# Performance work log

Measured on AMD Instinct MI355X. Metric: run time of the kernel, lower is better.

The kernel has to match this reference:

```python
import jax, jax.numpy as jnp
import numpy as np

N_NODES = 20000
N_EDGES = 200000
N_GRAPHS = 128
EMB = 256
N_LAYERS = 4
NUM_ELEMENTS = 84
RBF_DIM = 10
RBF_CUTOFF = 8.0


def setup_inputs() -> dict:
    key = jax.random.key(0)
    ks = jax.random.split(key, 20)
    inp = {
        'x': jax.random.randint(ks[0], (N_NODES, 1), 0, NUM_ELEMENTS, dtype=jnp.int64) if jax.config.read('jax_enable_x64') else jax.random.randint(ks[0], (N_NODES, 1), 0, NUM_ELEMENTS).astype(jnp.int32),
        'src': jax.random.randint(ks[1], (N_EDGES,), 0, N_NODES).astype(jnp.int32),
        'dst': jax.random.randint(ks[2], (N_EDGES,), 0, N_NODES).astype(jnp.int32),
        'e': jax.random.uniform(ks[3], (N_EDGES, 1), dtype=jnp.float32) * RBF_CUTOFF,
        'i': jnp.sort(jax.random.randint(ks[4], (N_NODES,), 0, N_GRAPHS)).astype(jnp.int32),
    }
    s_emb = 1.0 / np.sqrt(EMB)
    # element embedding table
    inp['emb_table'] = jax.random.normal(ks[5], (NUM_ELEMENTS, EMB), jnp.float32) * s_emb
    # dense_e applied to RBF expansion
    inp['We'] = jax.random.normal(ks[6], (RBF_DIM, EMB), jnp.float32) * (1.0 / np.sqrt(RBF_DIM))
    inp['be'] = jnp.zeros((EMB,), jnp.float32)
    # CGCNN-style gated message passing layers (stacked over layers)
    def w(k):
        return jax.random.normal(k, (N_LAYERS, EMB, EMB), jnp.float32) * s_emb
    inp['Wg_x'] = w(ks[7]); inp['Wg_n'] = w(ks[8]); inp['Wg_e'] = w(ks[9])
    inp['bg'] = jnp.zeros((N_LAYERS, EMB), jnp.float32)
    inp['Wf_x'] = w(ks[10]); inp['Wf_n'] = w(ks[11]); inp['Wf_e'] = w(ks[12])
    inp['bf'] = jnp.zeros((N_LAYERS, EMB), jnp.float32)
    # dense_n: embedding -> 12
    inp['Wn'] = jax.random.normal(ks[13], (EMB, 12), jnp.float32) * s_emb
    inp['bn'] = jnp.zeros((12,), jnp.float32)
    return inp


def _rbf_expand(d):
    # Gaussian radial basis expansion of scalar distances: [E] -> [E, RBF_DIM]
    centers = jnp.linspace(0.0, RBF_CUTOFF, RBF_DIM, dtype=d.dtype)
    width = centers[1] - centers[0]
    return jnp.exp(-(((d[:, None] - centers) / width) ** 2))


def reference(x, src, dst, e, i, emb_table, We, be, Wg_x, Wg_n, Wg_e, bg,
              Wf_x, Wf_n, Wf_e, bf, Wn, bn):
    xn = emb_table[x[:, 0]]                     # [N, EMB] element embedding
    ef = _rbf_expand(e[:, 0]) @ We + be         # [E, EMB] edge features
    for l in range(N_LAYERS):
        h_i = xn[dst]                           # receiver node features [E, EMB]
        h_j = xn[src]                           # sender node features   [E, EMB]
        # gate/filter computed as split matmuls (equivalent to Dense on concat)
        zg = h_i @ Wg_x[l] + h_j @ Wg_n[l] + ef @ Wg_e[l] + bg[l]
        zf = h_i @ Wf_x[l] + h_j @ Wf_n[l] + ef @ Wf_e[l] + bf[l]
        msg = jax.nn.sigmoid(zg) * jax.nn.softplus(zf)   # [E, EMB]
        agg = jax.ops.segment_sum(msg, dst, num_segments=N_NODES)
        xn = agg + xn                           # residual add (in model call)
    xs = xn @ Wn + bn                           # [N, 12]
    sums = jax.ops.segment_sum(xs, i, num_segments=N_GRAPHS)
    cnts = jax.ops.segment_sum(jnp.ones((xs.shape[0], 1), xs.dtype), i,
                               num_segments=N_GRAPHS)
    out = sums / jnp.maximum(cnts, 1.0)         # global average pool per graph
    return out.reshape(N_GRAPHS, 3, 4)
```

## Files before the change

### kernel.cpp

```cpp
#include <hip/hip_runtime.h>
#include <hip/hip_bf16.h>
#include <math.h>

#define NN   20000
#define NE   200000
#define NG   128
#define EMBD 256
#define NL   4
#define RBFD 10
#define TBINS 1024
#define NWAVE 8192
#define GSPL 8

typedef __attribute__((ext_vector_type(8))) short bf16x8;
typedef __attribute__((ext_vector_type(4))) float f32x4;

__device__ __forceinline__ f32x4 up4(uint2 u) {
  f32x4 r;
  r.x = __uint_as_float(u.x << 16);
  r.y = __uint_as_float(u.x & 0xffff0000u);
  r.z = __uint_as_float(u.y << 16);
  r.w = __uint_as_float(u.y & 0xffff0000u);
  return r;
}

__device__ __forceinline__ void gload16(const void* g, void* l) {
  __builtin_amdgcn_global_load_lds(
      (const __attribute__((address_space(1))) void*)g,
      (__attribute__((address_space(3))) void*)l, 16, 0, 0);
}

__device__ __forceinline__ unsigned short bfbits(float v) {
  __hip_bfloat16 h = __float2bfloat16(v);
  return *(unsigned short*)&h;
}


__global__ void k_embed(const int* __restrict__ x, const float* __restrict__ emb,
                        float* __restrict__ xn, __hip_bfloat16* __restrict__ xnb) {
  int idx = blockIdx.x * blockDim.x + threadIdx.x;
  if (idx >= NN * (EMBD / 4)) return;
  int n  = idx >> 6;
  int c4 = (idx & 63) << 2;
  float4 v = *(const float4*)(emb + (size_t)x[n] * EMBD + c4);
  *(float4*)(xn + (size_t)n * EMBD + c4) = v;
  __hip_bfloat16* xb = xnb + (size_t)n * EMBD + c4;
  xb[0] = __float2bfloat16(v.x); xb[1] = __float2bfloat16(v.y);
  xb[2] = __float2bfloat16(v.z); xb[3] = __float2bfloat16(v.w);
}

__global__ void k_wsmall(const float* __restrict__ We, const float* __restrict__ be,
                         const float* __restrict__ Wge, const float* __restrict__ bg,
                         const float* __restrict__ Wfe, const float* __restrict__ bf,
                         float* __restrict__ weff, float* __restrict__ beff) {
  int tid = blockIdx.x * blockDim.x + threadIdx.x;
  const int WPER = RBFD * EMBD;
  if (tid < NL * 2 * WPER) {
    int l  = tid / (2 * WPER);
    int r  = tid % (2 * WPER);
    int gf = r / WPER;
    int r2 = r % WPER;
    int k = r2 / EMBD, c = r2 % EMBD;
    const float* W = (gf == 0 ? Wge : Wfe) + (size_t)l * EMBD * EMBD;
    float s = 0.f;
    for (int j = 0; j < EMBD; ++j) s += We[k * EMBD + j] * W[(size_t)j * EMBD + c];
    weff[tid] = s;
  } else {
    int t2 = tid - NL * 2 * WPER;
    if (t2 >= NL * 2 * EMBD) return;
    int l  = t2 / (2 * EMBD);
    int r  = t2 % (2 * EMBD);
    int gf = r / EMBD, c = r % EMBD;
    const float* W = (gf == 0 ? Wge : Wfe) + (size_t)l * EMBD * EMBD;
    const float* b = (gf == 0 ? bg : bf) + (size_t)l * EMBD;
    float s = b[c];
    for (int j = 0; j < EMBD; ++j) s += be[j] * W[(size_t)j * EMBD + c];
    beff[t2] = s;
  }
}

__global__ void k_table(const float* __restrict__ weff, const float* __restrict__ beff,
                        float* __restrict__ tbl) {
  int idx = blockIdx.x * blockDim.x + threadIdx.x;
  if (idx >= NL * (TBINS + 1) * 512) return;
  int l = idx / ((TBINS + 1) * 512);
  int r = idx % ((TBINS + 1) * 512);
  int bin = r >> 9;
  int t = r & 511;
  int gf = t >> 8, c = t & 255;
  float d = (float)bin * (8.0f / (float)TBINS);
  const float* w = weff + ((size_t)(l * 2 + gf) * RBFD) * EMBD + c;
  float s = beff[(size_t)(l * 2 + gf) * EMBD + c];
  const float width = 8.0f / 9.0f;
  #pragma unroll
  for (int k = 0; k < RBFD; ++k) {
    float u = (d - (float)k * width) / width;
    s += __expf(-u * u) * w[(size_t)k * EMBD];
  }
  tbl[idx] = s;
}

__global__ __launch_bounds__(256) void k_wprep(
    const float* __restrict__ Wgx, const float* __restrict__ Wfx,
    const float* __restrict__ Wgn, const float* __restrict__ Wfn,
    __hip_bfloat16* __restrict__ WT) {
  __shared__ float T[64][65];
  int lq = blockIdx.x; int l = lq >> 2, q = lq & 3;
  const float* W = (q == 0 ? Wgx : q == 1 ? Wfx : q == 2 ? Wgn : Wfn) + (size_t)l * 65536;
  int t = blockIdx.y;
  int k0 = (t & 3) * 64, c0 = (t >> 2) * 64;
  #pragma unroll
  for (int i = 0; i < 16; ++i) {
    int idx = threadIdx.x + i * 256;
    int r = idx >> 6, c = idx & 63;
    T[r][c] = W[(size_t)(k0 + r) * 256 + c0 + c];
  }
  __syncthreads();
  __hip_bfloat16* out = WT + ((size_t)lq * 256) * 256;
  #pragma unroll
  for (int i = 0; i < 16; ++i) {
    int idx = threadIdx.x + i * 256;
    int r = idx >> 6, c = idx & 63;
    out[(size_t)(c0 + r) * 256 + k0 + c] = __float2bfloat16(T[c][r]);
  }
}


__global__ void k_hist(const int* __restrict__ dst, int* __restrict__ cnt) {
  int e = blockIdx.x * blockDim.x + threadIdx.x;
  if (e >= NE) return;
  atomicAdd(&cnt[dst[e]], 1);
}

__global__ __launch_bounds__(1024) void k_scan(const int* __restrict__ cnt,
                                               int* __restrict__ roff,
                                               int* __restrict__ cursor) {
  __shared__ int part[1024];
  const int t = threadIdx.x;
  const int CH = 20;
  int base = t * CH;
  int loc[CH];
  int s = 0;
  #pragma unroll
  for (int i = 0; i < CH; ++i) {
    int idx = base + i;
    int v = (idx < NN) ? cnt[idx] : 0;
    loc[i] = s;
    s += v;
  }
  part[t] = s;
  __syncthreads();
  for (int off = 1; off < 1024; off <<= 1) {
    int v = (t >= off) ? part[t - off] : 0;
    __syncthreads();
    part[t] += v;
    __syncthreads();
  }
  int chunkbase = (t == 0) ? 0 : part[t - 1];
  #pragma unroll
  for (int i = 0; i < CH; ++i) {
    int idx = base + i;
    if (idx < NN) {
      int v = chunkbase + loc[i];
      roff[idx] = v;
      cursor[idx] = v;
    }
  }
  if (t == 1023) roff[NN] = part[1023];
}

__global__ void k_scatter(const int* __restrict__ src, const int* __restrict__ dst,
                          const float* __restrict__ edist,
                          int* __restrict__ cursor,
                          int* __restrict__ src_s, float* __restrict__ db_s) {
  int e = blockIdx.x * blockDim.x + threadIdx.x;
  if (e >= NE) return;
  int d = dst[e];
  int p = atomicAdd(&cursor[d], 1);
  src_s[p] = src[e];
  float dd = edist[e] * ((float)TBINS / 8.0f);
  db_s[p] = fminf(fmaxf(dd, 0.0f), (float)TBINS - 0.001f);
}


__global__ __launch_bounds__(256) void k_nodemm(
    const __hip_bfloat16* __restrict__ xnb, const __hip_bfloat16* __restrict__ WTl,
    __hip_bfloat16* __restrict__ Yb) {
  __shared__ unsigned short As[128 * 64];
  __shared__ unsigned short Bs[128 * 64];
  const int tid = threadIdx.x;
  const int lane = tid & 63;
  const int wave = tid >> 6;
  const int row0 = blockIdx.x << 7;
  const int col0 = blockIdx.y << 7;
  const int q = col0 >> 8;
  const int cb = col0 & 255;
  const unsigned short* xb = (const unsigned short*)xnb;
  const unsigned short* Wb = (const unsigned short*)WTl + ((size_t)q * 256 + cb) * 256;
  const int wnode = (wave >> 1) << 6;
  const int wch   = (wave & 1) << 6;
  f32x4 acc[4][4] = {};

  const int rd0 = (wave << 3) + (lane >> 3);
  const int cd  = lane & 7;

  for (int k0 = 0; k0 < 256; k0 += 64) {
    #pragma unroll
    for (int j = 0; j < 4; ++j) {
      int rd = rd0 + j * 32;
      int cs = cd ^ (rd & 7);
      int ga = row0 + rd; if (ga > NN - 1) ga = NN - 1;
      gload16(xb + (size_t)ga * 256 + k0 + cs * 8,
              (char*)As + (size_t)(j * 256 + wave * 64) * 16);
      gload16(Wb + (size_t)rd * 256 + k0 + cs * 8,
              (char*)Bs + (size_t)(j * 256 + wave * 64) * 16);
    }
    __syncthreads();
    const int rsel = lane & 15, ksl = lane >> 4;
    #pragma unroll
    for (int h = 0; h < 2; ++h) {
      const int c = h * 4 + ksl;
      bf16x8 xa[4], wf[4];
      #pragma unroll
      for (int nn = 0; nn < 4; ++nn) {
        int r = wnode + nn * 16 + rsel;
        xa[nn] = *(const bf16x8*)(&As[r * 64 + (c ^ (r & 7)) * 8]);
      }
      #pragma unroll
      for (int mc = 0; mc < 4; ++mc) {
        int r = wch + mc * 16 + rsel;
        wf[mc] = *(const bf16x8*)(&Bs[r * 64 + (c ^ (r & 7)) * 8]);
      }
      #pragma unroll
      for (int mc = 0; mc < 4; ++mc)
        #pragma unroll
        for (int nn = 0; nn < 4; ++nn)
          acc[mc][nn] = __builtin_amdgcn_mfma_f32_16x16x32_bf16(wf[mc], xa[nn], acc[mc][nn], 0, 0, 0);
    }
    __syncthreads();
  }

  const int nodesel = lane & 15;
  const int chq = (lane >> 4) << 2;
  #pragma unroll
  for (int mc = 0; mc < 4; ++mc) {
    #pragma unroll
    for (int nn = 0; nn < 4; ++nn) {
      int node = row0 + wnode + nn * 16 + nodesel;
      if (node < NN) {
        int ch = col0 + wch + mc * 16 + chq;
        ushort4 pk;
        pk.x = bfbits(acc[mc][nn][0]);
        pk.y = bfbits(acc[mc][nn][1]);
        pk.z = bfbits(acc[mc][nn][2]);
        pk.w = bfbits(acc[mc][nn][3]);
        *(ushort4*)((unsigned short*)Yb + (size_t)node * 1024 + ch) = pk;
      }
    }
  }
}

__device__ __forceinline__ float gate1(float zg, float zf) {
  float sg = __builtin_amdgcn_rcpf(1.0f + __expf(-zg));
  float sp = fmaxf(zf, 0.0f) + __logf(1.0f + __expf(-fabsf(zf)));
  return sg * sp;
}

__global__ __launch_bounds__(256, 8) void k_agg(
    const __hip_bfloat16* __restrict__ Yb, const int* __restrict__ roff,
    const int* __restrict__ src_s, const float* __restrict__ db_s,
    const float* __restrict__ tblL,
    float* __restrict__ xn, __hip_bfloat16* __restrict__ xnb) {
  const int wave = threadIdx.x >> 6, lane = threadIdx.x & 63;
  const int c4 = lane << 2;
  const int wid0 = blockIdx.x * 4 + wave;

  for (int n = wid0; n < NN; n += NWAVE) {
    const int jb   = __builtin_amdgcn_readfirstlane(roff[n]);
    const int jend = __builtin_amdgcn_readfirstlane(roff[n + 1]);
    const int deg = jend - jb;

    const unsigned short* yrow = (const unsigned short*)Yb + (size_t)n * 1024 + c4;
    f32x4 bgv = up4(*(const uint2*)(yrow));
    f32x4 bfv = up4(*(const uint2*)(yrow + 256));

    f32x4 m4 = {};
    if (deg > 0) {
      const int dcap = deg < 64 ? deg : 64;
      int sv = 0; int bv = 0; int fv = 0;
      if (lane < dcap) {
        sv = src_s[jb + lane];
        float db = db_s[jb + lane];
        int b = (int)db;
        bv = b;
        fv = __float_as_int(db - (float)b);
      }
      const unsigned short* Ysrc = (const unsigned short*)Yb + c4 + 512;
      for (int i = 0; i < dcap; ++i) {
        int sn = __builtin_amdgcn_readlane(sv, i);
        int bn = __builtin_amdgcn_readlane(bv, i);
        float fr = __int_as_float(__builtin_amdgcn_readlane(fv, i));
        const unsigned short* ys = Ysrc + (size_t)sn * 1024;
        uint2 pa = *(const uint2*)(ys);
        uint2 pf = *(const uint2*)(ys + 256);
        const float* tp = tblL + (size_t)bn * 512 + c4;
        f32x4 t0g = *(const f32x4*)(tp);
        f32x4 t0f = *(const f32x4*)(tp + 256);
        f32x4 t1g = *(const f32x4*)(tp + 512);
        f32x4 t1f = *(const f32x4*)(tp + 768);
        f32x4 zg = bgv + up4(pa) + t0g + fr * (t1g - t0g);
        f32x4 zf = bfv + up4(pf) + t0f + fr * (t1f - t0f);
        m4.x += gate1(zg.x, zf.x);
        m4.y += gate1(zg.y, zf.y);
        m4.z += gate1(zg.z, zf.z);
        m4.w += gate1(zg.w, zf.w);
      }
      for (int i = 64; i < deg; ++i) {
        int sn = src_s[jb + i];
        float db = db_s[jb + i];
        int bn = (int)db;
        float fr = db - (float)bn;
        const unsigned short* ys = Ysrc + (size_t)sn * 1024;
        uint2 pa = *(const uint2*)(ys);
        uint2 pf = *(const uint2*)(ys + 256);
        const float* tp = tblL + (size_t)bn * 512 + c4;
        f32x4 t0g = *(const f32x4*)(tp);
        f32x4 t0f = *(const f32x4*)(tp + 256);
        f32x4 t1g = *(const f32x4*)(tp + 512);
        f32x4 t1f = *(const f32x4*)(tp + 768);
        f32x4 zg = bgv + up4(pa) + t0g + fr * (t1g - t0g);
        f32x4 zf = bfv + up4(pf) + t0f + fr * (t1f - t0f);
        m4.x += gate1(zg.x, zf.x);
        m4.y += gate1(zg.y, zf.y);
        m4.z += gate1(zg.z, zf.z);
        m4.w += gate1(zg.w, zf.w);
      }
    }
    float4 xv = *(const float4*)(xn + (size_t)n * EMBD + c4);
    xv.x += m4.x; xv.y += m4.y; xv.z += m4.z; xv.w += m4.w;
    *(float4*)(xn + (size_t)n * EMBD + c4) = xv;
    __hip_bfloat16* xbp = xnb + (size_t)n * EMBD + c4;
    xbp[0] = __float2bfloat16(xv.x); xbp[1] = __float2bfloat16(xv.y);
    xbp[2] = __float2bfloat16(xv.z); xbp[3] = __float2bfloat16(xv.w);
  }
}


__global__ __launch_bounds__(256) void k_gsum(
    const float* __restrict__ xn, const int* __restrict__ gi,
    float* __restrict__ gpart, float* __restrict__ gcnt) {
  const int g = blockIdx.x, p = blockIdx.y;
  int lo = 0, hi = NN;
  while (lo < hi) { int m = (lo + hi) >> 1; if (gi[m] < g) lo = m + 1; else hi = m; }
  int lo2 = lo, hi2 = NN;
  while (lo2 < hi2) { int m = (lo2 + hi2) >> 1; if (gi[m] < g + 1) lo2 = m + 1; else hi2 = m; }
  const int cntv = lo2 - lo;
  const int r0 = lo + (cntv * p) / GSPL;
  const int r1 = lo + (cntv * (p + 1)) / GSPL;
  const int c = threadIdx.x;
  float acc = 0.f;
  for (int r = r0; r < r1; ++r) acc += xn[(size_t)r * EMBD + c];
  gpart[((size_t)g * GSPL + p) * EMBD + c] = acc;
  if (p == 0 && c == 0) gcnt[g] = (float)cntv;
}

__global__ __launch_bounds__(256) void k_final(
    const float* __restrict__ gpart, const float* __restrict__ gcnt,
    const float* __restrict__ Wn, const float* __restrict__ bn,
    float* __restrict__ out) {
  __shared__ float s[EMBD];
  const int g = blockIdx.x;
  const int c = threadIdx.x;
  float v = 0.f;
  #pragma unroll
  for (int p = 0; p < GSPL; ++p) v += gpart[((size_t)g * GSPL + p) * EMBD + c];
  s[c] = v;
  __syncthreads();
  if (c < 12) {
    float acc = 0.f;
    for (int k = 0; k < EMBD; ++k) acc += s[k] * Wn[k * 12 + c];
    float cv = gcnt[g];
    out[g * 12 + c] = (cv > 0.f) ? acc / cv + bn[c] : 0.f;
  }
}


extern "C" void kernel_launch(void* const* d_in, const int* in_sizes, int n_in,
                              void* d_out, int out_size, void* d_ws, size_t ws_size,
                              hipStream_t stream) {
  const int*   x   = (const int*)d_in[0];
  const int*   src = (const int*)d_in[1];
  const int*   dst = (const int*)d_in[2];
  const float* e   = (const float*)d_in[3];
  const int*   gi  = (const int*)d_in[4];
  const float* emb = (const float*)d_in[5];
  const float* We  = (const float*)d_in[6];
  const float* be  = (const float*)d_in[7];
  const float* Wgx = (const float*)d_in[8];
  const float* Wgn = (const float*)d_in[9];
  const float* Wge = (const float*)d_in[10];
  const float* bg  = (const float*)d_in[11];
  const float* Wfx = (const float*)d_in[12];
  const float* Wfn = (const float*)d_in[13];
  const float* Wfe = (const float*)d_in[14];
  const float* bf  = (const float*)d_in[15];
  const float* Wn  = (const float*)d_in[16];
  const float* bn  = (const float*)d_in[17];
  float* out = (float*)d_out;

  char* ws = (char*)d_ws;
  size_t off = 0;
  auto alloc = [&](size_t bytes) {
    void* p = ws + off;
    off += (bytes + 255) & ~(size_t)255;
    return p;
  };
  float*           xn    = (float*)alloc((size_t)NN * EMBD * 4);
  __hip_bfloat16*  xnb   = (__hip_bfloat16*)alloc((size_t)NN * EMBD * 2);
  __hip_bfloat16*  Yb    = (__hip_bfloat16*)alloc((size_t)NN * 1024 * 2);
  float*           db_s  = (float*)alloc((size_t)NE * 4);
  int*             src_s = (int*)alloc((size_t)NE * 4);
  int*             cnt   = (int*)alloc((size_t)NN * 4);
  int*             roff  = (int*)alloc((size_t)(NN + 1) * 4);
  int*             curs  = (int*)alloc((size_t)NN * 4);
  float*           weff  = (float*)alloc((size_t)NL * 2 * RBFD * EMBD * 4);
  float*           beff  = (float*)alloc((size_t)NL * 2 * EMBD * 4);
  float*           tbl   = (float*)alloc((size_t)NL * (TBINS + 1) * 512 * 4);
  __hip_bfloat16*  WT    = (__hip_bfloat16*)alloc((size_t)NL * 4 * 256 * 256 * 2);
  float*           gpart = (float*)alloc((size_t)NG * GSPL * EMBD * 4);
  float*           gcnt  = (float*)alloc((size_t)NG * 4);
  (void)ws_size; (void)in_sizes; (void)n_in; (void)out_size;

  hipMemsetAsync(cnt, 0, (size_t)NN * 4, stream);

  k_embed<<<(NN * (EMBD / 4) + 255) / 256, 256, 0, stream>>>(x, emb, xn, xnb);
  k_wsmall<<<(NL * 2 * (RBFD + 1) * EMBD + 255) / 256, 256, 0, stream>>>(
      We, be, Wge, bg, Wfe, bf, weff, beff);
  k_table<<<(NL * (TBINS + 1) * 512 + 255) / 256, 256, 0, stream>>>(weff, beff, tbl);
  k_wprep<<<dim3(NL * 4, 16), 256, 0, stream>>>(Wgx, Wfx, Wgn, Wfn, WT);
  k_hist<<<(NE + 255) / 256, 256, 0, stream>>>(dst, cnt);
  k_scan<<<1, 1024, 0, stream>>>(cnt, roff, curs);
  k_scatter<<<(NE + 255) / 256, 256, 0, stream>>>(src, dst, e, curs, src_s, db_s);

  dim3 mmgrid((NN + 127) / 128, 8);
  for (int l = 0; l < NL; ++l) {
    k_nodemm<<<mmgrid, 256, 0, stream>>>(xnb, WT + (size_t)l * 4 * 65536, Yb);
    k_agg<<<NWAVE / 4, 256, 0, stream>>>(
        Yb, roff, src_s, db_s, tbl + (size_t)l * (TBINS + 1) * 512, xn, xnb);
  }
  k_gsum<<<dim3(NG, GSPL), 256, 0, stream>>>(xn, gi, gpart, gcnt);
  k_final<<<NG, 256, 0, stream>>>(gpart, gcnt, Wn, bn, out);
}
```

Baseline: 488.5 us.

## Use nearest-bin bf16 RBF table and atomic work-stealing in aggregation

The RBF edge-feature lookup table is stored in bf16 with twice as many bins, and edges look up the nearest bin instead of linearly interpolating between two fp32 bins. This drops two of four table loads per edge and halves the table bytes, cutting memory traffic in the aggregation kernel. The aggregation also replaces its static node-strided loop with a per-layer atomic counter so waves grab nodes dynamically to balance uneven degrees. The cost is lower accuracy from bf16 storage and nearest-bin quantisation, plus one atomic per node.

```diff
diff --git a/kernel.cpp b/kernel.cpp
--- a/kernel.cpp
+++ b/kernel.cpp
@@ -8,7 +8,7 @@
 #define EMBD 256
 #define NL   4
 #define RBFD 10
-#define TBINS 1024
+#define TBINS 2048
 #define NWAVE 8192
 #define GSPL 8
 
@@ -80,7 +80,7 @@
 }
 
 __global__ void k_table(const float* __restrict__ weff, const float* __restrict__ beff,
-                        float* __restrict__ tbl) {
+                        __hip_bfloat16* __restrict__ tbl) {
   int idx = blockIdx.x * blockDim.x + threadIdx.x;
   if (idx >= NL * (TBINS + 1) * 512) return;
   int l = idx / ((TBINS + 1) * 512);
@@ -97,7 +97,7 @@
     float u = (d - (float)k * width) / width;
     s += __expf(-u * u) * w[(size_t)k * EMBD];
   }
-  tbl[idx] = s;
+  tbl[idx] = __float2bfloat16(s);
 }
 
 __global__ __launch_bounds__(256) void k_wprep(
@@ -172,14 +172,15 @@
 __global__ void k_scatter(const int* __restrict__ src, const int* __restrict__ dst,
                           const float* __restrict__ edist,
                           int* __restrict__ cursor,
-                          int* __restrict__ src_s, float* __restrict__ db_s) {
+                          int* __restrict__ src_s, int* __restrict__ bin_s) {
   int e = blockIdx.x * blockDim.x + threadIdx.x;
   if (e >= NE) return;
   int d = dst[e];
   int p = atomicAdd(&cursor[d], 1);
   src_s[p] = src[e];
-  float dd = edist[e] * ((float)TBINS / 8.0f);
-  db_s[p] = fminf(fmaxf(dd, 0.0f), (float)TBINS - 0.001f);
+  int bin = (int)(edist[e] * ((float)TBINS / 8.0f) + 0.5f);
+  bin = bin < 0 ? 0 : (bin > TBINS ? TBINS : bin);
+  bin_s[p] = bin << 9;
 }
 
 
@@ -268,48 +269,48 @@
 
 __global__ __launch_bounds__(256, 8) void k_agg(
     const __hip_bfloat16* __restrict__ Yb, const int* __restrict__ roff,
-    const int* __restrict__ src_s, const float* __restrict__ db_s,
-    const float* __restrict__ tblL,
-    float* __restrict__ xn, __hip_bfloat16* __restrict__ xnb) {
-  const int wave = threadIdx.x >> 6, lane = threadIdx.x & 63;
+    const int* __restrict__ src_s, const int* __restrict__ bin_s,
+    const __hip_bfloat16* __restrict__ tblL,
+    float* __restrict__ xn, __hip_bfloat16* __restrict__ xnb,
+    int* __restrict__ ctr) {
+  const int lane = threadIdx.x & 63;
   const int c4 = lane << 2;
-  const int wid0 = blockIdx.x * 4 + wave;
-
-  for (int n = wid0; n < NN; n += NWAVE) {
+  const unsigned short* Ybu = (const unsigned short*)Yb;
+  const unsigned short* Tbu = (const unsigned short*)tblL;
+
+  for (;;) {
+    int grab = 0;
+    if (lane == 0) grab = atomicAdd(ctr, 1);
+    const int n = __builtin_amdgcn_readfirstlane(grab);
+    if (n >= NN) break;
+
     const int jb   = __builtin_amdgcn_readfirstlane(roff[n]);
     const int jend = __builtin_amdgcn_readfirstlane(roff[n + 1]);
     const int deg = jend - jb;
 
-    const unsigned short* yrow = (const unsigned short*)Yb + (size_t)n * 1024 + c4;
-    f32x4 bgv = up4(*(const uint2*)(yrow));
-    f32x4 bfv = up4(*(const uint2*)(yrow + 256));
+    const unsigned short* yr = Ybu + (size_t)n * 1024;
+    f32x4 bgv = up4(*(const uint2*)(yr + c4));
+    f32x4 bfv = up4(*(const uint2*)(yr + c4 + 256));
 
     f32x4 m4 = {};
     if (deg > 0) {
       const int dcap = deg < 64 ? deg : 64;
-      int sv = 0; int bv = 0; int fv = 0;
+      int sv = 0, bv = 0;
       if (lane < dcap) {
         sv = src_s[jb + lane];
-        float db = db_s[jb + lane];
-        int b = (int)db;
-        bv = b;
-        fv = __float_as_int(db - (float)b);
-      }
-      const unsigned short* Ysrc = (const unsigned short*)Yb + c4 + 512;
+        bv = bin_s[jb + lane];
+      }
       for (int i = 0; i < dcap; ++i) {
         int sn = __builtin_amdgcn_readlane(sv, i);
-        int bn = __builtin_amdgcn_readlane(bv, i);
-        float fr = __int_as_float(__builtin_amdgcn_readlane(fv, i));
-        const unsigned short* ys = Ysrc + (size_t)sn * 1024;
-        uint2 pa = *(const uint2*)(ys);
-        uint2 pf = *(const uint2*)(ys + 256);
-        const float* tp = tblL + (size_t)bn * 512 + c4;
-        f32x4 t0g = *(const f32x4*)(tp);
-        f32x4 t0f = *(const f32x4*)(tp + 256);
-        f32x4 t1g = *(const f32x4*)(tp + 512);
-        f32x4 t1f = *(const f32x4*)(tp + 768);
-        f32x4 zg = bgv + up4(pa) + t0g + fr * (t1g - t0g);
-        f32x4 zf = bfv + up4(pf) + t0f + fr * (t1f - t0f);
+        int bo = __builtin_amdgcn_readlane(bv, i);
+        const unsigned short* ys = Ybu + (size_t)sn * 1024 + 512;
+        uint2 pa = *(const uint2*)(ys + c4);
+        uint2 pf = *(const uint2*)(ys + c4 + 256);
+        const unsigned short* tp = Tbu + bo;
+        uint2 tg = *(const uint2*)(tp + c4);
+        uint2 tf = *(const uint2*)(tp + c4 + 256);
+        f32x4 zg = bgv + up4(pa) + up4(tg);
+        f32x4 zf = bfv + up4(pf) + up4(tf);
         m4.x += gate1(zg.x, zf.x);
         m4.y += gate1(zg.y, zf.y);
         m4.z += gate1(zg.z, zf.z);
@@ -317,19 +318,15 @@
       }
       for (int i = 64; i < deg; ++i) {
         int sn = src_s[jb + i];
-        float db = db_s[jb + i];
-        int bn = (int)db;
-        float fr = db - (float)bn;
-        const unsigned short* ys = Ysrc + (size_t)sn * 1024;
-        uint2 pa = *(const uint2*)(ys);
-        uint2 pf = *(const uint2*)(ys + 256);
-        const float* tp = tblL + (size_t)bn * 512 + c4;
-        f32x4 t0g = *(const f32x4*)(tp);
-        f32x4 t0f = *(const f32x4*)(tp + 256);
-        f32x4 t1g = *(const f32x4*)(tp + 512);
-        f32x4 t1f = *(const f32x4*)(tp + 768);
-        f32x4 zg = bgv + up4(pa) + t0g + fr * (t1g - t0g);
-        f32x4 zf = bfv + up4(pf) + t0f + fr * (t1f - t0f);
+        int bo = bin_s[jb + i];
+        const unsigned short* ys = Ybu + (size_t)sn * 1024 + 512;
+        uint2 pa = *(const uint2*)(ys + c4);
+        uint2 pf = *(const uint2*)(ys + c4 + 256);
+        const unsigned short* tp = Tbu + bo;
+        uint2 tg = *(const uint2*)(tp + c4);
+        uint2 tf = *(const uint2*)(tp + c4 + 256);
+        f32x4 zg = bgv + up4(pa) + up4(tg);
+        f32x4 zf = bfv + up4(pf) + up4(tf);
         m4.x += gate1(zg.x, zf.x);
         m4.y += gate1(zg.y, zf.y);
         m4.z += gate1(zg.z, zf.z);
@@ -418,20 +415,22 @@
   float*           xn    = (float*)alloc((size_t)NN * EMBD * 4);
   __hip_bfloat16*  xnb   = (__hip_bfloat16*)alloc((size_t)NN * EMBD * 2);
   __hip_bfloat16*  Yb    = (__hip_bfloat16*)alloc((size_t)NN * 1024 * 2);
-  float*           db_s  = (float*)alloc((size_t)NE * 4);
+  int*             bin_s = (int*)alloc((size_t)NE * 4);
   int*             src_s = (int*)alloc((size_t)NE * 4);
   int*             cnt   = (int*)alloc((size_t)NN * 4);
   int*             roff  = (int*)alloc((size_t)(NN + 1) * 4);
   int*             curs  = (int*)alloc((size_t)NN * 4);
   float*           weff  = (float*)alloc((size_t)NL * 2 * RBFD * EMBD * 4);
   float*           beff  = (float*)alloc((size_t)NL * 2 * EMBD * 4);
-  float*           tbl   = (float*)alloc((size_t)NL * (TBINS + 1) * 512 * 4);
+  __hip_bfloat16*  tbl   = (__hip_bfloat16*)alloc((size_t)NL * (TBINS + 1) * 512 * 2);
   __hip_bfloat16*  WT    = (__hip_bfloat16*)alloc((size_t)NL * 4 * 256 * 256 * 2);
   float*           gpart = (float*)alloc((size_t)NG * GSPL * EMBD * 4);
   float*           gcnt  = (float*)alloc((size_t)NG * 4);
+  int*             ctr   = (int*)alloc((size_t)NL * 4);
   (void)ws_size; (void)in_sizes; (void)n_in; (void)out_size;
 
   hipMemsetAsync(cnt, 0, (size_t)NN * 4, stream);
+  hipMemsetAsync(ctr, 0, (size_t)NL * 4, stream);
 
   k_embed<<<(NN * (EMBD / 4) + 255) / 256, 256, 0, stream>>>(x, emb, xn, xnb);
   k_wsmall<<<(NL * 2 * (RBFD + 1) * EMBD + 255) / 256, 256, 0, stream>>>(
@@ -440,13 +439,13 @@
   k_wprep<<<dim3(NL * 4, 16), 256, 0, stream>>>(Wgx, Wfx, Wgn, Wfn, WT);
   k_hist<<<(NE + 255) / 256, 256, 0, stream>>>(dst, cnt);
   k_scan<<<1, 1024, 0, stream>>>(cnt, roff, curs);
-  k_scatter<<<(NE + 255) / 256, 256, 0, stream>>>(src, dst, e, curs, src_s, db_s);
+  k_scatter<<<(NE + 255) / 256, 256, 0, stream>>>(src, dst, e, curs, src_s, bin_s);
 
   dim3 mmgrid((NN + 127) / 128, 8);
   for (int l = 0; l < NL; ++l) {
     k_nodemm<<<mmgrid, 256, 0, stream>>>(xnb, WT + (size_t)l * 4 * 65536, Yb);
     k_agg<<<NWAVE / 4, 256, 0, stream>>>(
-        Yb, roff, src_s, db_s, tbl + (size_t)l * (TBINS + 1) * 512, xn, xnb);
+        Yb, roff, src_s, bin_s, tbl + (size_t)l * (TBINS + 1) * 512, xn, xnb, ctr + l);
   }
   k_gsum<<<dim3(NG, GSPL), 256, 0, stream>>>(xn, gi, gpart, gcnt);
   k_final<<<NG, 256, 0, stream>>>(gpart, gcnt, Wn, bn, out);
```

New measurement: 1.579 ms. 223% more time.
